# Optimization experiments

Hardware: AMD Instinct MI355X
Metric: run time of the kernel (lower is better)

## Reference

```python
import jax, jax.numpy as jnp
import numpy as np

N, E, G = 50000, 800000, 64          # nodes, edges, graphs in batch
H, C = 4, 32                          # heads, per-head channels
D = H * C                             # 128 = gat_hidden_dim * n_heads
EMB = 16
IN_DIM = 2 * EMB + 1                  # 33
LSTM_H = 256
OUT = 4
V_LAB, V_TYP = 1000, 100
EPS = 1e-5


def _gatv2(x, src, dst, Wl, bl, Wr, br, att, bias):
    # GATv2Conv (PyG semantics, self-loops already appended to src/dst).
    xl = (x @ Wl + bl).reshape(-1, H, C)   # lin_l -> source-side messages x_j
    xr = (x @ Wr + br).reshape(-1, H, C)   # lin_r -> target-side x_i
    xj = xl[src]                            # [Et, H, C]
    e = jax.nn.leaky_relu(xr[dst] + xj, 0.2)
    score = jnp.einsum('ehc,hc->eh', e, att)             # [Et, H]
    smax = jax.ops.segment_max(score, dst, num_segments=N)
    a = jnp.exp(score - smax[dst])
    denom = jax.ops.segment_sum(a, dst, num_segments=N)
    alpha = a / denom[dst]                                # scatter-softmax per dst
    out = jax.ops.segment_sum(xj * alpha[:, :, None], dst, num_segments=N)
    return out.reshape(N, D) + bias


def _graph_norm(x, batch_ids, w, b, ms):
    # PyG GraphNorm: per-graph mean (scaled by learnable ms) and variance.
    cnt = jax.ops.segment_sum(jnp.ones((N,), x.dtype), batch_ids, num_segments=G)[:, None]
    mean = jax.ops.segment_sum(x, batch_ids, num_segments=G) / cnt
    out = x - mean[batch_ids] * ms
    var = jax.ops.segment_sum(out * out, batch_ids, num_segments=G) / cnt
    return w * out / jnp.sqrt(var + EPS)[batch_ids] + b


def _lstm0(x, Wih, Whh, bih, bhh):
    # Single LSTM time-step with h0 = c0 = 0: the Whh @ h0 term vanishes,
    # the forget gate multiplies c0 = 0.  Gate order (PyTorch): i, f, g, o.
    g = x @ Wih.T + bih + bhh
    i, f, gg, o = jnp.split(g, 4, axis=-1)
    c = jax.nn.sigmoid(i) * jnp.tanh(gg)
    return jax.nn.sigmoid(o) * jnp.tanh(c)


def setup_inputs() -> dict:
    key = jax.random.key(0)
    ks = jax.random.split(key, 32)
    rn = lambda k, s, sc=0.05: jax.random.normal(k, s, jnp.float32) * sc
    Z4 = LSTM_H * 4
    return {
        'node_labels': jax.random.randint(ks[0], (N,), 0, V_LAB, jnp.int32),
        'node_types': jax.random.randint(ks[1], (N,), 0, V_TYP, jnp.int32),
        'node_feat': jax.random.normal(ks[2], (N, 1), jnp.float32),
        'edge_index': jax.random.randint(ks[3], (2, E), 0, N, jnp.int32),
        'batch_ids': jnp.sort(jax.random.randint(ks[4], (N,), 0, G, jnp.int32)),
        'emb_label': rn(ks[5], (V_LAB, EMB), 1.0),
        'emb_type': rn(ks[6], (V_TYP, EMB), 1.0),
        'W_in': rn(ks[7], (IN_DIM, D)), 'b_in': jnp.zeros((D,), jnp.float32),
        'g1_Wl': rn(ks[8], (D, D)), 'g1_bl': jnp.zeros((D,), jnp.float32),
        'g1_Wr': rn(ks[9], (D, D)), 'g1_br': jnp.zeros((D,), jnp.float32),
        'g1_att': rn(ks[10], (H, C), 0.1), 'g1_bias': jnp.zeros((D,), jnp.float32),
        'gn1_w': jnp.ones((D,), jnp.float32), 'gn1_b': jnp.zeros((D,), jnp.float32),
        'gn1_ms': jnp.ones((D,), jnp.float32),
        'g2_Wl': rn(ks[11], (D, D)), 'g2_bl': jnp.zeros((D,), jnp.float32),
        'g2_Wr': rn(ks[12], (D, D)), 'g2_br': jnp.zeros((D,), jnp.float32),
        'g2_att': rn(ks[13], (H, C), 0.1), 'g2_bias': jnp.zeros((D,), jnp.float32),
        'gn2_w': jnp.ones((D,), jnp.float32), 'gn2_b': jnp.zeros((D,), jnp.float32),
        'gn2_ms': jnp.ones((D,), jnp.float32),
        'W_res': rn(ks[14], (D, D)), 'b_res': jnp.zeros((D,), jnp.float32),
        'l1_Wih': rn(ks[15], (Z4, D)), 'l1_Whh': rn(ks[16], (Z4, LSTM_H)),
        'l1_bih': jnp.zeros((Z4,), jnp.float32), 'l1_bhh': jnp.zeros((Z4,), jnp.float32),
        'l2_Wih': rn(ks[17], (Z4, LSTM_H)), 'l2_Whh': rn(ks[18], (Z4, LSTM_H)),
        'l2_bih': jnp.zeros((Z4,), jnp.float32), 'l2_bhh': jnp.zeros((Z4,), jnp.float32),
        'ln_w': jnp.ones((LSTM_H,), jnp.float32), 'ln_b': jnp.zeros((LSTM_H,), jnp.float32),
        'fc_W': rn(ks[19], (LSTM_H, OUT)), 'fc_b': jnp.zeros((OUT,), jnp.float32),
    }


def reference(node_labels, node_types, node_feat, edge_index, batch_ids,
              emb_label, emb_type, W_in, b_in,
              g1_Wl, g1_bl, g1_Wr, g1_br, g1_att, g1_bias, gn1_w, gn1_b, gn1_ms,
              g2_Wl, g2_bl, g2_Wr, g2_br, g2_att, g2_bias, gn2_w, gn2_b, gn2_ms,
              W_res, b_res,
              l1_Wih, l1_Whh, l1_bih, l1_bhh, l2_Wih, l2_Whh, l2_bih, l2_bhh,
              ln_w, ln_b, fc_W, fc_b):
    # Node features: [label_emb | type_emb | scalar]  -> [N, 33]
    feat = jnp.concatenate([emb_label[node_labels], emb_type[node_types], node_feat], axis=1)
    # PositionalEncoding at position 0 with odd d_model=33 adds exactly zeros (no-op).
    x = feat @ W_in + b_in                                  # [N, D]

    loops = jnp.arange(N, dtype=edge_index.dtype)           # GATv2Conv add_self_loops=True
    src = jnp.concatenate([edge_index[0], loops])
    dst = jnp.concatenate([edge_index[1], loops])

    x1 = jax.nn.elu(_graph_norm(_gatv2(x, src, dst, g1_Wl, g1_bl, g1_Wr, g1_br, g1_att, g1_bias),
                                batch_ids, gn1_w, gn1_b, gn1_ms))
    # dropout = identity in eval mode
    x2 = jax.nn.elu(_graph_norm(_gatv2(x1, src, dst, g2_Wl, g2_bl, g2_Wr, g2_br, g2_att, g2_bias),
                                batch_ids, gn2_w, gn2_b, gn2_ms) + x1 @ W_res + b_res)

    h1 = _lstm0(x2, l1_Wih, l1_Whh, l1_bih, l1_bhh)         # seq_len = 1 LSTM
    h2 = _lstm0(h1, l2_Wih, l2_Whh, l2_bih, l2_bhh)

    mu = h2.mean(-1, keepdims=True)
    var = ((h2 - mu) ** 2).mean(-1, keepdims=True)
    hn = ln_w * (h2 - mu) / jnp.sqrt(var + EPS) + ln_b      # LayerNorm

    cnt = jax.ops.segment_sum(jnp.ones((N,), hn.dtype), batch_ids, num_segments=G)[:, None]
    pooled = jax.ops.segment_sum(hn, batch_ids, num_segments=G) / cnt  # global_mean_pool
    return jax.nn.log_softmax(pooled @ fc_W + fc_b, axis=1)            # [G, OUT]
```

## Files before the change

### kernel.cpp

```cpp
#include <hip/hip_runtime.h>
#include <cstdint>
#include <cstddef>

#define DD 128
#define LSTMH 256
#define ZG 1024

typedef __attribute__((ext_vector_type(8))) short short8v;
typedef __attribute__((ext_vector_type(4))) float float4v;

static inline int cdiv_(int a, int b) { return (a + b - 1) / b; }

__device__ __forceinline__ float sigm_(float x) { return 1.f / (1.f + __expf(-x)); }
__device__ __forceinline__ float tanh_(float x) {
  float e = __expf(-2.f * fabsf(x));
  float r = (1.f - e) / (1.f + e);
  return copysignf(r, x);
}

__device__ __forceinline__ unsigned short f2bf(float f) {
  uint32_t u = __float_as_uint(f);
  u += 0x7fffu + ((u >> 16) & 1u);
  return (unsigned short)(u >> 16);
}
__device__ __forceinline__ float bflo(uint32_t u) { return __uint_as_float(u << 16); }
__device__ __forceinline__ float bfhi(uint32_t u) { return __uint_as_float(u & 0xffff0000u); }
__device__ __forceinline__ float bfu(unsigned short u) { return __uint_as_float((uint32_t)u << 16); }

__global__ void cvt_direct(const float* __restrict__ W, unsigned short* __restrict__ o, int n) {
  int i = blockIdx.x * 256 + threadIdx.x;
  if (i < n) o[i] = f2bf(W[i]);
}

__global__ void cvt_transpose(const float* __restrict__ W, unsigned short* __restrict__ o,
                              int K, int M) {
  int i = blockIdx.x * 256 + threadIdx.x;
  if (i >= K * M) return;
  int m = i / K, k = i - m * K;
  o[i] = f2bf(W[(size_t)k * M + m]);
}

__global__ void prep_small(const float* g1bl, const float* g1br, const float* g2bl,
                           const float* g2br, const float* bres, const float* l1bih,
                           const float* l1bhh, const float* l2bih, const float* l2bhh,
                           float* bcat1, float* bcat2, float* bsum1, float* bsum2) {
  int t = blockIdx.x * 256 + threadIdx.x;
  if (t < 256) bcat1[t] = t < 128 ? g1bl[t] : g1br[t - 128];
  if (t < 384) bcat2[t] = t < 128 ? g2bl[t] : (t < 256 ? g2br[t - 128] : bres[t - 256]);
  if (t < ZG) { bsum1[t] = l1bih[t] + l1bhh[t]; bsum2[t] = l2bih[t] + l2bhh[t]; }
}

__global__ __launch_bounds__(128) void embed_in(
    const int* __restrict__ labels, const int* __restrict__ types,
    const float* __restrict__ nf, const float* __restrict__ embL,
    const float* __restrict__ embT, const float* __restrict__ W,
    const float* __restrict__ b, unsigned short* __restrict__ x, int N) {
  int n = blockIdx.x;
  if (n >= N) return;
  int t = threadIdx.x;
  __shared__ float f[33];
  if (t < 16) f[t] = embL[labels[n] * 16 + t];
  else if (t < 32) f[t] = embT[types[n] * 16 + (t - 16)];
  else if (t == 32) f[32] = nf[n];
  __syncthreads();
  float acc = b[t];
#pragma unroll
  for (int k = 0; k < 33; ++k) acc += f[k] * W[k * DD + t];
  x[(size_t)n * DD + t] = f2bf(acc);
}

__global__ void count_deg(const int* __restrict__ ei, int* __restrict__ deg, int E_, int N_) {
  int i = blockIdx.x * 256 + threadIdx.x;
  if (i < E_) atomicAdd(&deg[ei[E_ + i]], 1);
  else if (i < E_ + N_) atomicAdd(&deg[i - E_], 1);
}

__global__ __launch_bounds__(256) void scan1(const int* __restrict__ deg, int* __restrict__ offs,
                                             int* __restrict__ partials, int N_) {
  __shared__ int buf[2][256];
  int tid = threadIdx.x;
  int i = blockIdx.x * 256 + tid;
  int v = (i < N_) ? deg[i] : 0;
  buf[0][tid] = v;
  __syncthreads();
  int cur = 0;
#pragma unroll
  for (int d = 1; d < 256; d <<= 1) {
    int xv = buf[cur][tid];
    if (tid >= d) xv += buf[cur][tid - d];
    buf[cur ^ 1][tid] = xv;
    cur ^= 1;
    __syncthreads();
  }
  int incl = buf[cur][tid];
  if (i < N_) offs[i] = incl - v;
  if (tid == 255) partials[blockIdx.x] = incl;
}

__global__ __launch_bounds__(256) void scan2(int* __restrict__ partials, int* __restrict__ offs,
                                             int nb, int N_) {
  __shared__ int buf[2][256];
  int tid = threadIdx.x;
  int v = (tid < nb) ? partials[tid] : 0;
  buf[0][tid] = v;
  __syncthreads();
  int cur = 0;
#pragma unroll
  for (int d = 1; d < 256; d <<= 1) {
    int xv = buf[cur][tid];
    if (tid >= d) xv += buf[cur][tid - d];
    buf[cur ^ 1][tid] = xv;
    cur ^= 1;
    __syncthreads();
  }
  int incl = buf[cur][tid];
  if (tid < nb) partials[tid] = incl - v;
  if (tid == 255) offs[N_] = incl;
}

__global__ void scan3(int* __restrict__ offs, const int* __restrict__ partials, int N_) {
  int i = blockIdx.x * 256 + threadIdx.x;
  if (i < N_) offs[i] += partials[blockIdx.x];
}

__global__ void fill_csr(const int* __restrict__ ei, const int* __restrict__ offs,
                         int* __restrict__ cursor, int* __restrict__ csr, int E_, int N_) {
  int i = blockIdx.x * 256 + threadIdx.x;
  int s, d;
  if (i < E_) { s = ei[i]; d = ei[E_ + i]; }
  else if (i < E_ + N_) { s = d = i - E_; }
  else return;
  int pos = offs[d] + atomicAdd(&cursor[d], 1);
  csr[pos] = s;
}

__global__ void graph_ranges(const int* __restrict__ bids, int* __restrict__ gstart,
                             float* __restrict__ invcnt, int N_, int G_) {
  int t = threadIdx.x;
  if (t <= G_) {
    int lo = 0, hi = N_;
    while (lo < hi) { int mid = (lo + hi) >> 1; if (bids[mid] < t) lo = mid + 1; else hi = mid; }
    gstart[t] = lo;
  }
  __syncthreads();
  if (t < G_) {
    int c = gstart[t + 1] - gstart[t];
    invcnt[t] = (c > 0) ? 1.f / (float)c : 0.f;
  }
}

__global__ __launch_bounds__(256) void gemm_bf16(
    const unsigned short* __restrict__ A, const unsigned short* __restrict__ Bp,
    const float* __restrict__ bias, unsigned short* __restrict__ C, int M, int K, int Ncols) {
  __shared__ unsigned short As[128 * 40];
  __shared__ unsigned short Bs[128 * 40];
  int tid = threadIdx.x;
  int lane = tid & 63;
  int wid = tid >> 6;
  int rowBase = blockIdx.y * 128, colBase = blockIdx.x * 128;
  int wr = (wid >> 1) * 64, wc = (wid & 1) * 64;
  int fr = lane & 15, fg = lane >> 4;
  float4v acc[4][4];
#pragma unroll
  for (int i = 0; i < 4; ++i)
#pragma unroll
    for (int j = 0; j < 4; ++j) acc[i][j] = (float4v){0.f, 0.f, 0.f, 0.f};

  int sr = tid >> 2;
  int sc = tid & 3;
  int off_lo = (sc < 2) ? 32 * sc : 32 * sc - 56;

  for (int k0 = 0; k0 < K; k0 += 32) {
#pragma unroll
    for (int it = 0; it < 2; ++it) {
      int r = it * 64 + sr;
      uint4 va = make_uint4(0u, 0u, 0u, 0u);
      if (rowBase + r < M)
        va = *(const uint4*)(A + (size_t)(rowBase + r) * K + k0 + sc * 8);
      char* arow = (char*)(As + r * 40);
      *(uint2*)(arow + off_lo) = make_uint2(va.x, va.y);
      *(uint2*)(arow + off_lo + 16) = make_uint2(va.z, va.w);
      uint4 vb = *(const uint4*)(Bp + (size_t)(colBase + r) * K + k0 + sc * 8);
      char* brow = (char*)(Bs + r * 40);
      *(uint2*)(brow + off_lo) = make_uint2(vb.x, vb.y);
      *(uint2*)(brow + off_lo + 16) = make_uint2(vb.z, vb.w);
    }
    __syncthreads();
    short8v af[4], bfv[4];
#pragma unroll
    for (int i = 0; i < 4; ++i)
      af[i] = *(const short8v*)((const char*)As + (wr + 16 * i + fr) * 80 + fg * 16);
#pragma unroll
    for (int j = 0; j < 4; ++j)
      bfv[j] = *(const short8v*)((const char*)Bs + (wc + 16 * j + fr) * 80 + fg * 16);
#pragma unroll
    for (int i = 0; i < 4; ++i)
#pragma unroll
      for (int j = 0; j < 4; ++j)
        acc[i][j] = __builtin_amdgcn_mfma_f32_16x16x32_bf16(af[i], bfv[j], acc[i][j], 0, 0, 0);
    __syncthreads();
  }
#pragma unroll
  for (int j = 0; j < 4; ++j) {
    int gc = colBase + wc + 16 * j + fr;
    float bv = bias[gc];
#pragma unroll
    for (int i = 0; i < 4; ++i) {
      int gr0 = rowBase + wr + 16 * i + fg * 4;
#pragma unroll
      for (int rg = 0; rg < 4; ++rg) {
        int gr = gr0 + rg;
        if (gr < M) C[(size_t)gr * Ncols + gc] = f2bf(acc[i][j][rg] + bv);
      }
    }
  }
}

__global__ __launch_bounds__(256) void gat_agg(
    const unsigned short* __restrict__ xlr, int stride,
    const int* __restrict__ csr, const int* __restrict__ offs,
    const float* __restrict__ att, const float* __restrict__ bias,
    float* __restrict__ out, int N) {
  int wid = (blockIdx.x * 256 + threadIdx.x) >> 6;
  if (wid >= N) return;
  int lane = threadIdx.x & 63;
  int q = lane >> 4, ql = lane & 15;
  float4 aA = *(const float4*)&att[ql * 8];
  float4 aB = *(const float4*)&att[ql * 8 + 4];
  uint4 ur = *(const uint4*)(xlr + (size_t)wid * stride + 128 + ql * 8);
  float r0 = bflo(ur.x), r1 = bfhi(ur.x), r2 = bflo(ur.y), r3 = bfhi(ur.y);
  float r4 = bflo(ur.z), r5 = bfhi(ur.z), r6 = bflo(ur.w), r7 = bfhi(ur.w);
  float m = -1e30f, L = 0.f;
  float s0 = 0.f, s1 = 0.f, s2 = 0.f, s3 = 0.f, s4 = 0.f, s5 = 0.f, s6 = 0.f, s7 = 0.f;
  int js = offs[wid], je = offs[wid + 1];
  for (int j = js + q; j < je; j += 4) {
    int s = csr[j];
    uint4 u = *(const uint4*)(xlr + (size_t)s * stride + ql * 8);
    float x0 = bflo(u.x), x1 = bfhi(u.x), x2 = bflo(u.y), x3 = bfhi(u.y);
    float x4 = bflo(u.z), x5 = bfhi(u.z), x6 = bflo(u.w), x7 = bfhi(u.w);
    float v0 = fmaxf(r0 + x0, 0.2f * (r0 + x0));
    float v1 = fmaxf(r1 + x1, 0.2f * (r1 + x1));
    float v2 = fmaxf(r2 + x2, 0.2f * (r2 + x2));
    float v3 = fmaxf(r3 + x3, 0.2f * (r3 + x3));
    float v4 = fmaxf(r4 + x4, 0.2f * (r4 + x4));
    float v5 = fmaxf(r5 + x5, 0.2f * (r5 + x5));
    float v6 = fmaxf(r6 + x6, 0.2f * (r6 + x6));
    float v7 = fmaxf(r7 + x7, 0.2f * (r7 + x7));
    float p = aA.x * v0 + aA.y * v1 + aA.z * v2 + aA.w * v3 +
              aB.x * v4 + aB.y * v5 + aB.z * v6 + aB.w * v7;
    p += __shfl_xor(p, 1); p += __shfl_xor(p, 2);
    p += __shfl_xor(p, 4); p += __shfl_xor(p, 8);
    float mn = fmaxf(m, p);
    float ea = __expf(p - mn);
    float es = __expf(m - mn);
    L = L * es + ea;
    s0 = s0 * es + ea * x0; s1 = s1 * es + ea * x1;
    s2 = s2 * es + ea * x2; s3 = s3 * es + ea * x3;
    s4 = s4 * es + ea * x4; s5 = s5 * es + ea * x5;
    s6 = s6 * es + ea * x6; s7 = s7 * es + ea * x7;
    m = mn;
  }
#pragma unroll
  for (int d = 16; d <= 32; d <<= 1) {
    float mo = __shfl_xor(m, d), Lo = __shfl_xor(L, d);
    float t0 = __shfl_xor(s0, d), t1 = __shfl_xor(s1, d);
    float t2 = __shfl_xor(s2, d), t3 = __shfl_xor(s3, d);
    float t4 = __shfl_xor(s4, d), t5 = __shfl_xor(s5, d);
    float t6 = __shfl_xor(s6, d), t7 = __shfl_xor(s7, d);
    float mn = fmaxf(m, mo);
    float e0 = __expf(m - mn), e1 = __expf(mo - mn);
    L = L * e0 + Lo * e1;
    s0 = s0 * e0 + t0 * e1; s1 = s1 * e0 + t1 * e1;
    s2 = s2 * e0 + t2 * e1; s3 = s3 * e0 + t3 * e1;
    s4 = s4 * e0 + t4 * e1; s5 = s5 * e0 + t5 * e1;
    s6 = s6 * e0 + t6 * e1; s7 = s7 * e0 + t7 * e1;
    m = mn;
  }
  if (q == 0) {
    float inv = 1.f / L;
    float4 bA = *(const float4*)&bias[ql * 8];
    float4 bB = *(const float4*)&bias[ql * 8 + 4];
    float4 oA, oB;
    oA.x = s0 * inv + bA.x; oA.y = s1 * inv + bA.y;
    oA.z = s2 * inv + bA.z; oA.w = s3 * inv + bA.w;
    oB.x = s4 * inv + bB.x; oB.y = s5 * inv + bB.y;
    oB.z = s6 * inv + bB.z; oB.w = s7 * inv + bB.w;
    *(float4*)&out[(size_t)wid * DD + ql * 8] = oA;
    *(float4*)&out[(size_t)wid * DD + ql * 8 + 4] = oB;
  }
}

__global__ __launch_bounds__(256) void gn_stats2(const float* __restrict__ x,
                                                 const int* __restrict__ bids,
                                                 float* __restrict__ gsum,
                                                 float* __restrict__ gsq, int N) {
  int base = blockIdx.x * 128;
  int ch = threadIdx.x & 127;
  int sub = threadIdx.x >> 7;
  int end = base + 128 < N ? base + 128 : N;
  int curg = -1;
  float s = 0.f, q = 0.f;
  for (int r = base + sub; r < end; r += 2) {
    int g = bids[r];
    if (g != curg) {
      if (curg >= 0) {
        atomicAdd(&gsum[curg * DD + ch], s);
        atomicAdd(&gsq[curg * DD + ch], q);
      }
      curg = g; s = 0.f; q = 0.f;
    }
    float v = x[(size_t)r * DD + ch];
    s += v; q += v * v;
  }
  if (curg >= 0) {
    atomicAdd(&gsum[curg * DD + ch], s);
    atomicAdd(&gsq[curg * DD + ch], q);
  }
}

template <bool ADDRES>
__global__ void gn_apply(const float* __restrict__ xin, unsigned short* __restrict__ xout,
                         const unsigned short* __restrict__ res, int resStride,
                         const int* __restrict__ bids, const float* __restrict__ gsum,
                         const float* __restrict__ gsq, const float* __restrict__ invcnt,
                         const float* __restrict__ w, const float* __restrict__ b,
                         const float* __restrict__ ms, int N) {
  int idx = blockIdx.x * 256 + threadIdx.x;
  if (idx >= N * DD) return;
  int n = idx >> 7, ch = idx & 127;
  int g = bids[n];
  float ic = invcnt[g];
  float mean = gsum[g * DD + ch] * ic;
  float ex2 = gsq[g * DD + ch] * ic;
  float mm = mean * ms[ch];
  float var = ex2 - mm * (2.f * mean - mm);
  float v = (xin[idx] - mm) * rsqrtf(var + 1e-5f) * w[ch] + b[ch];
  if (ADDRES) v += bfu(res[(size_t)n * resStride + ch]);
  v = v > 0.f ? v : (__expf(v) - 1.f);
  xout[idx] = f2bf(v);
}

template <int KD>
__global__ __launch_bounds__(256) void lstm_big(
    const unsigned short* __restrict__ A, const unsigned short* __restrict__ Bp,
    const float* __restrict__ bsum, unsigned short* __restrict__ H, int M) {
  __shared__ __attribute__((aligned(16))) char As_[128 * 272];
  __shared__ __attribute__((aligned(16))) char Ws_[96 * 272];
  int npanel = (M + 127) >> 7;
  int b = blockIdx.x;
  int g8 = b & 7, inner = b >> 3;
  int p = g8 + 8 * (inner >> 3);
  int cc = inner & 7;
  if (p >= npanel) return;
  int rowBase = p << 7;
  int ch0 = cc * 32;

  int tid = threadIdx.x;
  int lane = tid & 63;
  int wid = tid >> 6;
  int wr2 = wid >> 1, wc2 = wid & 1;
  int fr = lane & 15, fg = lane >> 4;

  float4v acc[4][3];
#pragma unroll
  for (int i = 0; i < 4; ++i)
#pragma unroll
    for (int j = 0; j < 3; ++j) acc[i][j] = (float4v){0.f, 0.f, 0.f, 0.f};

#pragma unroll
  for (int ph = 0; ph < KD / 128; ++ph) {
    int koff = ph * 128;
    if (ph) __syncthreads();
#pragma unroll
    for (int q = 0; q < 8; ++q) {
      int t = q * 256 + tid;
      int r = t >> 4, c = (t >> 2) & 3, sc = t & 3;
      uint4 va = make_uint4(0u, 0u, 0u, 0u);
      int gr = rowBase + r;
      if (gr < M) va = *(const uint4*)(A + (size_t)gr * KD + koff + c * 32 + sc * 8);
      int olo = (sc < 2) ? 32 * sc : 32 * sc - 56;
      char* dst = As_ + r * 272 + c * 64;
      *(uint2*)(dst + olo) = make_uint2(va.x, va.y);
      *(uint2*)(dst + olo + 16) = make_uint2(va.z, va.w);
    }
#pragma unroll
    for (int q = 0; q < 6; ++q) {
      int t = q * 256 + tid;
      int wrow = t >> 4, c = (t >> 2) & 3, sc = t & 3;
      int half = wrow >= 48 ? 1 : 0;
      int r3 = wrow - 48 * half;
      int grp = r3 >> 4;
      int goff = (grp == 0) ? 0 : (grp == 1 ? 512 : 768);
      int grow = goff + ch0 + 16 * half + (r3 & 15);
      uint4 vb = *(const uint4*)(Bp + (size_t)grow * KD + koff + c * 32 + sc * 8);
      int olo = (sc < 2) ? 32 * sc : 32 * sc - 56;
      char* dst = Ws_ + wrow * 272 + c * 64;
      *(uint2*)(dst + olo) = make_uint2(vb.x, vb.y);
      *(uint2*)(dst + olo + 16) = make_uint2(vb.z, vb.w);
    }
    __syncthreads();
#pragma unroll
    for (int c = 0; c < 4; ++c) {
      short8v af[4], bf[3];
#pragma unroll
      for (int i = 0; i < 4; ++i)
        af[i] = *(const short8v*)(As_ + (64 * wr2 + 16 * i + fr) * 272 + c * 64 + fg * 16);
#pragma unroll
      for (int j = 0; j < 3; ++j)
        bf[j] = *(const short8v*)(Ws_ + (48 * wc2 + 16 * j + fr) * 272 + c * 64 + fg * 16);
#pragma unroll
      for (int i = 0; i < 4; ++i)
#pragma unroll
        for (int j = 0; j < 3; ++j)
          acc[i][j] = __builtin_amdgcn_mfma_f32_16x16x32_bf16(af[i], bf[j], acc[i][j], 0, 0, 0);
    }
  }
  int ch = ch0 + 16 * wc2 + fr;
  float bi = bsum[ch], bg = bsum[512 + ch], bo = bsum[768 + ch];
#pragma unroll
  for (int i = 0; i < 4; ++i) {
#pragma unroll
    for (int rg = 0; rg < 4; ++rg) {
      int row = rowBase + 64 * wr2 + 16 * i + 4 * fg + rg;
      if (row < M) {
        float iv = acc[i][0][rg] + bi;
        float gv = acc[i][1][rg] + bg;
        float ov = acc[i][2][rg] + bo;
        float c = sigm_(iv) * tanh_(gv);
        H[(size_t)row * LSTMH + ch] = f2bf(sigm_(ov) * tanh_(c));
      }
    }
  }
}

__global__ __launch_bounds__(256) void ln_pool2(
    const unsigned short* __restrict__ h2, const int* __restrict__ bids,
    const float* __restrict__ lnw, const float* __restrict__ lnb,
    const float* __restrict__ invcnt, float* __restrict__ pooled, int N) {
  int wave = (blockIdx.x * 256 + threadIdx.x) >> 6;
  int lane = threadIdx.x & 63;
  int r0 = wave * 8;
  if (r0 >= N) return;
  float4 w4 = *(const float4*)&lnw[lane * 4];
  float4 b4 = *(const float4*)&lnb[lane * 4];
  float p0 = 0.f, p1 = 0.f, p2 = 0.f, p3 = 0.f;
  int curg = bids[r0];
  int rend = r0 + 8 < N ? r0 + 8 : N;
  for (int r = r0; r < rend; ++r) {
    int g = bids[r];
    if (g != curg) {
      float ic = invcnt[curg];
      atomicAdd(&pooled[curg * LSTMH + lane * 4 + 0], p0 * ic);
      atomicAdd(&pooled[curg * LSTMH + lane * 4 + 1], p1 * ic);
      atomicAdd(&pooled[curg * LSTMH + lane * 4 + 2], p2 * ic);
      atomicAdd(&pooled[curg * LSTMH + lane * 4 + 3], p3 * ic);
      p0 = p1 = p2 = p3 = 0.f;
      curg = g;
    }
    uint2 u = *(const uint2*)(h2 + (size_t)r * LSTMH + lane * 4);
    float v0 = bflo(u.x), v1 = bfhi(u.x), v2 = bflo(u.y), v3 = bfhi(u.y);
    float s = v0 + v1 + v2 + v3;
    float q = v0 * v0 + v1 * v1 + v2 * v2 + v3 * v3;
#pragma unroll
    for (int d = 1; d < 64; d <<= 1) { s += __shfl_xor(s, d); q += __shfl_xor(q, d); }
    float mu = s * (1.f / 256.f);
    float var = q * (1.f / 256.f) - mu * mu;
    float rs = rsqrtf(var + 1e-5f);
    p0 += w4.x * (v0 - mu) * rs + b4.x;
    p1 += w4.y * (v1 - mu) * rs + b4.y;
    p2 += w4.z * (v2 - mu) * rs + b4.z;
    p3 += w4.w * (v3 - mu) * rs + b4.w;
  }
  float ic = invcnt[curg];
  atomicAdd(&pooled[curg * LSTMH + lane * 4 + 0], p0 * ic);
  atomicAdd(&pooled[curg * LSTMH + lane * 4 + 1], p1 * ic);
  atomicAdd(&pooled[curg * LSTMH + lane * 4 + 2], p2 * ic);
  atomicAdd(&pooled[curg * LSTMH + lane * 4 + 3], p3 * ic);
}

__global__ __launch_bounds__(64) void fc_lsm(const float* __restrict__ pooled,
                                             const float* __restrict__ W,
                                             const float* __restrict__ b, float* __restrict__ out) {
  int g = blockIdx.x;
  int t = threadIdx.x;
  float l0 = 0.f, l1 = 0.f, l2 = 0.f, l3 = 0.f;
  for (int k = t; k < LSTMH; k += 64) {
    float p = pooled[g * LSTMH + k];
    l0 += p * W[k * 4 + 0];
    l1 += p * W[k * 4 + 1];
    l2 += p * W[k * 4 + 2];
    l3 += p * W[k * 4 + 3];
  }
#pragma unroll
  for (int d = 1; d < 64; d <<= 1) {
    l0 += __shfl_xor(l0, d); l1 += __shfl_xor(l1, d);
    l2 += __shfl_xor(l2, d); l3 += __shfl_xor(l3, d);
  }
  if (t == 0) {
    float z[4] = {l0 + b[0], l1 + b[1], l2 + b[2], l3 + b[3]};
    float mx = fmaxf(fmaxf(z[0], z[1]), fmaxf(z[2], z[3]));
    float sum = __expf(z[0] - mx) + __expf(z[1] - mx) + __expf(z[2] - mx) + __expf(z[3] - mx);
    float ls = logf(sum);
#pragma unroll
    for (int o = 0; o < 4; ++o) out[g * 4 + o] = z[o] - mx - ls;
  }
}

extern "C" void kernel_launch(void* const* d_in, const int* in_sizes, int n_in,
                              void* d_out, int out_size, void* d_ws, size_t ws_size,
                              hipStream_t stream) {
  const int* node_labels = (const int*)d_in[0];
  const int* node_types = (const int*)d_in[1];
  const float* node_feat = (const float*)d_in[2];
  const int* edge_index = (const int*)d_in[3];
  const int* batch_ids = (const int*)d_in[4];
  const float* emb_label = (const float*)d_in[5];
  const float* emb_type = (const float*)d_in[6];
  const float* W_in = (const float*)d_in[7];
  const float* b_in = (const float*)d_in[8];
  const float* g1_Wl = (const float*)d_in[9];
  const float* g1_bl = (const float*)d_in[10];
  const float* g1_Wr = (const float*)d_in[11];
  const float* g1_br = (const float*)d_in[12];
  const float* g1_att = (const float*)d_in[13];
  const float* g1_bias = (const float*)d_in[14];
  const float* gn1_w = (const float*)d_in[15];
  const float* gn1_b = (const float*)d_in[16];
  const float* gn1_ms = (const float*)d_in[17];
  const float* g2_Wl = (const float*)d_in[18];
  const float* g2_bl = (const float*)d_in[19];
  const float* g2_Wr = (const float*)d_in[20];
  const float* g2_br = (const float*)d_in[21];
  const float* g2_att = (const float*)d_in[22];
  const float* g2_bias = (const float*)d_in[23];
  const float* gn2_w = (const float*)d_in[24];
  const float* gn2_b = (const float*)d_in[25];
  const float* gn2_ms = (const float*)d_in[26];
  const float* W_res = (const float*)d_in[27];
  const float* b_res = (const float*)d_in[28];
  const float* l1_Wih = (const float*)d_in[29];
  const float* l1_bih = (const float*)d_in[31];
  const float* l1_bhh = (const float*)d_in[32];
  const float* l2_Wih = (const float*)d_in[33];
  const float* l2_bih = (const float*)d_in[35];
  const float* l2_bhh = (const float*)d_in[36];
  const float* ln_w = (const float*)d_in[37];
  const float* ln_b = (const float*)d_in[38];
  const float* fc_W = (const float*)d_in[39];
  const float* fc_b = (const float*)d_in[40];
  float* out = (float*)d_out;

  const int N = in_sizes[0];
  const int E = in_sizes[3] / 2;
  const int G = out_size / 4;
  const int ET = E + N;

  char* wsb = (char*)d_ws;
  size_t off = 0;
  auto alloc = [&](size_t bytes) -> void* {
    void* p = (void*)(wsb + off);
    off = (off + bytes + 255) & ~(size_t)255;
    return p;
  };
  float* xA = (float*)alloc((size_t)N * DD * 4);
  unsigned short* xb = (unsigned short*)alloc((size_t)N * DD * 2);
  unsigned short* xlr = (unsigned short*)alloc((size_t)N * 384 * 2);
  int* deg = (int*)alloc((size_t)N * 4);
  int* offs = (int*)alloc((size_t)(N + 1) * 4);
  int* cursor = (int*)alloc((size_t)N * 4);
  int* partials = (int*)alloc(1024);
  int* csr = (int*)alloc((size_t)ET * 4);
  int* gstart = (int*)alloc((size_t)(G + 1) * 4);
  float* invcnt = (float*)alloc((size_t)G * 4);
  float* gsum = (float*)alloc((size_t)G * DD * 4);
  float* gsq = (float*)alloc((size_t)G * DD * 4);
  float* pooled = (float*)alloc((size_t)G * LSTMH * 4);
  float* bcat1 = (float*)alloc(256 * 4);
  float* bcat2 = (float*)alloc(384 * 4);
  float* bsum1 = (float*)alloc(ZG * 4);
  float* bsum2 = (float*)alloc(ZG * 4);
  unsigned short* wcat1 = (unsigned short*)alloc((size_t)256 * DD * 2);
  unsigned short* wcat2 = (unsigned short*)alloc((size_t)384 * DD * 2);
  unsigned short* wl1b = (unsigned short*)alloc((size_t)ZG * DD * 2);
  unsigned short* wl2b = (unsigned short*)alloc((size_t)ZG * LSTMH * 2);
  (void)ws_size; (void)n_in;

  unsigned short* h1 = xlr;
  unsigned short* h2 = (unsigned short*)xA;

  hipMemsetAsync(deg, 0, (size_t)N * 4, stream);
  hipMemsetAsync(cursor, 0, (size_t)N * 4, stream);
  hipMemsetAsync(pooled, 0, (size_t)G * LSTMH * 4, stream);

  cvt_transpose<<<cdiv_(DD * DD, 256), 256, 0, stream>>>(g1_Wl, wcat1, DD, DD);
  cvt_transpose<<<cdiv_(DD * DD, 256), 256, 0, stream>>>(g1_Wr, wcat1 + DD * DD, DD, DD);
  cvt_transpose<<<cdiv_(DD * DD, 256), 256, 0, stream>>>(g2_Wl, wcat2, DD, DD);
  cvt_transpose<<<cdiv_(DD * DD, 256), 256, 0, stream>>>(g2_Wr, wcat2 + DD * DD, DD, DD);
  cvt_transpose<<<cdiv_(DD * DD, 256), 256, 0, stream>>>(W_res, wcat2 + 2 * DD * DD, DD, DD);
  cvt_direct<<<cdiv_(ZG * DD, 256), 256, 0, stream>>>(l1_Wih, wl1b, ZG * DD);
  cvt_direct<<<cdiv_(ZG * LSTMH, 256), 256, 0, stream>>>(l2_Wih, wl2b, ZG * LSTMH);
  prep_small<<<4, 256, 0, stream>>>(g1_bl, g1_br, g2_bl, g2_br, b_res, l1_bih, l1_bhh,
                                    l2_bih, l2_bhh, bcat1, bcat2, bsum1, bsum2);

  graph_ranges<<<1, 128, 0, stream>>>(batch_ids, gstart, invcnt, N, G);
  embed_in<<<N, 128, 0, stream>>>(node_labels, node_types, node_feat, emb_label, emb_type,
                                  W_in, b_in, xb, N);

  count_deg<<<cdiv_(ET, 256), 256, 0, stream>>>(edge_index, deg, E, N);
  int nb1 = cdiv_(N, 256);
  scan1<<<nb1, 256, 0, stream>>>(deg, offs, partials, N);
  scan2<<<1, 256, 0, stream>>>(partials, offs, nb1, N);
  scan3<<<nb1, 256, 0, stream>>>(offs, partials, N);
  fill_csr<<<cdiv_(ET, 256), 256, 0, stream>>>(edge_index, offs, cursor, csr, E, N);

  int mb = cdiv_(N, 128);
  gemm_bf16<<<dim3(2, mb), 256, 0, stream>>>(xb, wcat1, bcat1, xlr, N, DD, 256);
  gat_agg<<<cdiv_(N, 4), 256, 0, stream>>>(xlr, 256, csr, offs, g1_att, g1_bias, xA, N);
  hipMemsetAsync(gsum, 0, (size_t)G * DD * 8, stream);
  gn_stats2<<<cdiv_(N, 128), 256, 0, stream>>>(xA, batch_ids, gsum, gsq, N);
  gn_apply<false><<<cdiv_(N * DD, 256), 256, 0, stream>>>(
      xA, xb, nullptr, 0, batch_ids, gsum, gsq, invcnt, gn1_w, gn1_b, gn1_ms, N);
  gemm_bf16<<<dim3(3, mb), 256, 0, stream>>>(xb, wcat2, bcat2, xlr, N, DD, 384);
  gat_agg<<<cdiv_(N, 4), 256, 0, stream>>>(xlr, 384, csr, offs, g2_att, g2_bias, xA, N);
  hipMemsetAsync(gsum, 0, (size_t)G * DD * 8, stream);
  gn_stats2<<<cdiv_(N, 128), 256, 0, stream>>>(xA, batch_ids, gsum, gsq, N);
  gn_apply<true><<<cdiv_(N * DD, 256), 256, 0, stream>>>(
      xA, xb, xlr + 256, 384, batch_ids, gsum, gsq, invcnt, gn2_w, gn2_b, gn2_ms, N);
  int npanel = cdiv_(N, 128);
  int lblocks = 64 * cdiv_(npanel, 8);
  lstm_big<DD><<<lblocks, 256, 0, stream>>>(xb, wl1b, bsum1, h1, N);
  lstm_big<LSTMH><<<lblocks, 256, 0, stream>>>(h1, wl2b, bsum2, h2, N);
  ln_pool2<<<cdiv_(N, 32), 256, 0, stream>>>(h2, batch_ids, ln_w, ln_b, invcnt, pooled, N);
  fc_lsm<<<G, 64, 0, stream>>>(pooled, fc_W, fc_b, out);
}
```

Measured before the change: 569.5 us.

## Double the LSTM GEMM block to 512 threads with register prefetch and staged stores

The LSTM gate GEMM now runs 8 waves per block, each owning a 32x48 sub-tile instead of 64x48, which halves per-thread accumulators. Global loads for the next K-phase are prefetched into registers while the MFMAs for the current phase run. Output h values are staged through shared memory so each row is written with coalesced 16-byte stores instead of scattered 2-byte stores. In exchange it adds extra barriers and a redundant duplicated initial load loop, and relies on higher occupancy to hide latency.

Measured after the change: 533.6 us. -6.3%, faster.

```diff
diff --git a/kernel.cpp b/kernel.cpp
--- a/kernel.cpp
+++ b/kernel.cpp
@@ -341,11 +341,12 @@
 }
 
 template <int KD>
-__global__ __launch_bounds__(256) void lstm_big(
+__global__ __launch_bounds__(512, 4) void lstm_big(
     const unsigned short* __restrict__ A, const unsigned short* __restrict__ Bp,
     const float* __restrict__ bsum, unsigned short* __restrict__ H, int M) {
   __shared__ __attribute__((aligned(16))) char As_[128 * 272];
   __shared__ __attribute__((aligned(16))) char Ws_[96 * 272];
+  const int NPH = KD / 128;
   int npanel = (M + 127) >> 7;
   int b = blockIdx.x;
   int g8 = b & 7, inner = b >> 3;
@@ -358,77 +359,144 @@
   int tid = threadIdx.x;
   int lane = tid & 63;
   int wid = tid >> 6;
-  int wr2 = wid >> 1, wc2 = wid & 1;
+  int wr4 = wid >> 1;
+  int wc2 = wid & 1;
   int fr = lane & 15, fg = lane >> 4;
 
-  float4v acc[4][3];
-#pragma unroll
-  for (int i = 0; i < 4; ++i)
+  int ar[4], ac[4], aolo[4], aldst[4];
+#pragma unroll
+  for (int q = 0; q < 4; ++q) {
+    int e = q * 512 + tid;
+    int r = e >> 4, kk = e & 15;
+    int c = kk >> 2, sc = kk & 3;
+    ar[q] = r; ac[q] = c;
+    aolo[q] = (sc < 2) ? 32 * sc : 32 * sc - 56;
+    aldst[q] = r * 272 + c * 64;
+  }
+  int wgrow[3], wc_[3], wolo[3], wldst[3];
+#pragma unroll
+  for (int q = 0; q < 3; ++q) {
+    int e = q * 512 + tid;
+    int wrow = e >> 4, kk = e & 15;
+    int c = kk >> 2, sc = kk & 3;
+    int half = wrow >= 48 ? 1 : 0;
+    int r3 = wrow - 48 * half;
+    int grp = r3 >> 4;
+    int goff = (grp == 0) ? 0 : (grp == 1 ? 512 : 768);
+    wgrow[q] = goff + ch0 + 16 * half + (r3 & 15);
+    wc_[q] = c;
+    wolo[q] = (sc < 2) ? 32 * sc : 32 * sc - 56;
+    wldst[q] = wrow * 272 + c * 64;
+  }
+
+  float4v acc[2][3];
+#pragma unroll
+  for (int i = 0; i < 2; ++i)
 #pragma unroll
     for (int j = 0; j < 3; ++j) acc[i][j] = (float4v){0.f, 0.f, 0.f, 0.f};
 
-#pragma unroll
-  for (int ph = 0; ph < KD / 128; ++ph) {
-    int koff = ph * 128;
+  uint4 va[4], vw[3];
+#pragma unroll
+  for (int q = 0; q < 4; ++q) {
+    va[q] = make_uint4(0u, 0u, 0u, 0u);
+    if (rowBase + ar[q] < M)
+      va[q] = *(const uint4*)(A + (size_t)(rowBase + ar[q]) * KD + ac[q] * 32 + (aolo[q] == 32 || aolo[q] == 40 ? 0 : 0) + ((aolo[q] < 32) ? (aolo[q] >> 5) * 0 : 0) + 0 + ((q * 512 + tid) & 3) * 8);
+  }
+#pragma unroll
+  for (int q = 0; q < 4; ++q) {
+    int e = q * 512 + tid;
+    int sc = e & 3;
+    va[q] = make_uint4(0u, 0u, 0u, 0u);
+    if (rowBase + ar[q] < M)
+      va[q] = *(const uint4*)(A + (size_t)(rowBase + ar[q]) * KD + ac[q] * 32 + sc * 8);
+  }
+#pragma unroll
+  for (int q = 0; q < 3; ++q) {
+    int e = q * 512 + tid;
+    int sc = e & 3;
+    vw[q] = *(const uint4*)(Bp + (size_t)wgrow[q] * KD + wc_[q] * 32 + sc * 8);
+  }
+
+#pragma unroll
+  for (int ph = 0; ph < NPH; ++ph) {
     if (ph) __syncthreads();
 #pragma unroll
-    for (int q = 0; q < 8; ++q) {
-      int t = q * 256 + tid;
-      int r = t >> 4, c = (t >> 2) & 3, sc = t & 3;
-      uint4 va = make_uint4(0u, 0u, 0u, 0u);
-      int gr = rowBase + r;
-      if (gr < M) va = *(const uint4*)(A + (size_t)gr * KD + koff + c * 32 + sc * 8);
-      int olo = (sc < 2) ? 32 * sc : 32 * sc - 56;
-      char* dst = As_ + r * 272 + c * 64;
-      *(uint2*)(dst + olo) = make_uint2(va.x, va.y);
-      *(uint2*)(dst + olo + 16) = make_uint2(va.z, va.w);
-    }
-#pragma unroll
-    for (int q = 0; q < 6; ++q) {
-      int t = q * 256 + tid;
-      int wrow = t >> 4, c = (t >> 2) & 3, sc = t & 3;
-      int half = wrow >= 48 ? 1 : 0;
-      int r3 = wrow - 48 * half;
-      int grp = r3 >> 4;
-      int goff = (grp == 0) ? 0 : (grp == 1 ? 512 : 768);
-      int grow = goff + ch0 + 16 * half + (r3 & 15);
-      uint4 vb = *(const uint4*)(Bp + (size_t)grow * KD + koff + c * 32 + sc * 8);
-      int olo = (sc < 2) ? 32 * sc : 32 * sc - 56;
-      char* dst = Ws_ + wrow * 272 + c * 64;
-      *(uint2*)(dst + olo) = make_uint2(vb.x, vb.y);
-      *(uint2*)(dst + olo + 16) = make_uint2(vb.z, vb.w);
+    for (int q = 0; q < 4; ++q) {
+      char* dst = As_ + aldst[q];
+      *(uint2*)(dst + aolo[q]) = make_uint2(va[q].x, va[q].y);
+      *(uint2*)(dst + aolo[q] + 16) = make_uint2(va[q].z, va[q].w);
+    }
+#pragma unroll
+    for (int q = 0; q < 3; ++q) {
+      char* dst = Ws_ + wldst[q];
+      *(uint2*)(dst + wolo[q]) = make_uint2(vw[q].x, vw[q].y);
+      *(uint2*)(dst + wolo[q] + 16) = make_uint2(vw[q].z, vw[q].w);
     }
     __syncthreads();
+    if (ph + 1 < NPH) {
+      int koff = (ph + 1) * 128;
+#pragma unroll
+      for (int q = 0; q < 4; ++q) {
+        int e = q * 512 + tid;
+        int sc = e & 3;
+        va[q] = make_uint4(0u, 0u, 0u, 0u);
+        if (rowBase + ar[q] < M)
+          va[q] = *(const uint4*)(A + (size_t)(rowBase + ar[q]) * KD + koff + ac[q] * 32 + sc * 8);
+      }
+#pragma unroll
+      for (int q = 0; q < 3; ++q) {
+        int e = q * 512 + tid;
+        int sc = e & 3;
+        vw[q] = *(const uint4*)(Bp + (size_t)wgrow[q] * KD + koff + wc_[q] * 32 + sc * 8);
+      }
+    }
 #pragma unroll
     for (int c = 0; c < 4; ++c) {
-      short8v af[4], bf[3];
-#pragma unroll
-      for (int i = 0; i < 4; ++i)
-        af[i] = *(const short8v*)(As_ + (64 * wr2 + 16 * i + fr) * 272 + c * 64 + fg * 16);
+      short8v af[2], bf[3];
+#pragma unroll
+      for (int i = 0; i < 2; ++i)
+        af[i] = *(const short8v*)(As_ + (32 * wr4 + 16 * i + fr) * 272 + c * 64 + fg * 16);
 #pragma unroll
       for (int j = 0; j < 3; ++j)
         bf[j] = *(const short8v*)(Ws_ + (48 * wc2 + 16 * j + fr) * 272 + c * 64 + fg * 16);
 #pragma unroll
-      for (int i = 0; i < 4; ++i)
+      for (int i = 0; i < 2; ++i)
 #pragma unroll
         for (int j = 0; j < 3; ++j)
           acc[i][j] = __builtin_amdgcn_mfma_f32_16x16x32_bf16(af[i], bf[j], acc[i][j], 0, 0, 0);
     }
   }
-  int ch = ch0 + 16 * wc2 + fr;
+  int chL = 16 * wc2 + fr;
+  int ch = ch0 + chL;
   float bi = bsum[ch], bg = bsum[512 + ch], bo = bsum[768 + ch];
-#pragma unroll
-  for (int i = 0; i < 4; ++i) {
+  unsigned short hv[8];
+#pragma unroll
+  for (int i = 0; i < 2; ++i) {
 #pragma unroll
     for (int rg = 0; rg < 4; ++rg) {
-      int row = rowBase + 64 * wr2 + 16 * i + 4 * fg + rg;
-      if (row < M) {
-        float iv = acc[i][0][rg] + bi;
-        float gv = acc[i][1][rg] + bg;
-        float ov = acc[i][2][rg] + bo;
-        float c = sigm_(iv) * tanh_(gv);
-        H[(size_t)row * LSTMH + ch] = f2bf(sigm_(ov) * tanh_(c));
-      }
+      float iv = acc[i][0][rg] + bi;
+      float gv = acc[i][1][rg] + bg;
+      float ov = acc[i][2][rg] + bo;
+      float c = sigm_(iv) * tanh_(gv);
+      hv[i * 4 + rg] = f2bf(sigm_(ov) * tanh_(c));
+    }
+  }
+  __syncthreads();
+  unsigned short* Hs = (unsigned short*)As_;
+#pragma unroll
+  for (int i = 0; i < 2; ++i) {
+#pragma unroll
+    for (int rg = 0; rg < 4; ++rg) {
+      int row = 32 * wr4 + 16 * i + 4 * fg + rg;
+      Hs[row * 40 + chL] = hv[i * 4 + rg];
+    }
+  }
+  __syncthreads();
+  {
+    int row = tid >> 2, seg = tid & 3;
+    if (rowBase + row < M) {
+      uint4 v = *(const uint4*)(Hs + row * 40 + seg * 8);
+      *(uint4*)(H + (size_t)(rowBase + row) * LSTMH + ch0 + seg * 8) = v;
     }
   }
 }
@@ -628,8 +696,8 @@
       xA, xb, xlr + 256, 384, batch_ids, gsum, gsq, invcnt, gn2_w, gn2_b, gn2_ms, N);
   int npanel = cdiv_(N, 128);
   int lblocks = 64 * cdiv_(npanel, 8);
-  lstm_big<DD><<<lblocks, 256, 0, stream>>>(xb, wl1b, bsum1, h1, N);
-  lstm_big<LSTMH><<<lblocks, 256, 0, stream>>>(h1, wl2b, bsum2, h2, N);
+  lstm_big<DD><<<lblocks, 512, 0, stream>>>(xb, wl1b, bsum1, h1, N);
+  lstm_big<LSTMH><<<lblocks, 512, 0, stream>>>(h1, wl2b, bsum2, h2, N);
   ln_pool2<<<cdiv_(N, 32), 256, 0, stream>>>(h2, batch_ids, ln_w, ln_b, invcnt, pooled, N);
   fc_lsm<<<G, 64, 0, stream>>>(pooled, fc_W, fc_b, out);
 }
```
